# Kernel optimization log

Measured on AMD Instinct MI355X. Metric: run time of the kernel, lower is better.

## Reference

```python
import jax, jax.numpy as jnp
import numpy as np

B, TQ, TK, D, NA = 8, 512, 2048, 1024, 512
H, HD = 16, 64          # n_head, head_dim (D = H*HD)
NE, HID = 4, 32         # n_experts, expert hidden_dim
EPS = 1e-6


def _rmsnorm(x, w):
    return x * jax.lax.rsqrt(jnp.mean(x * x, axis=-1, keepdims=True) + EPS) * w


def setup_inputs() -> dict:
    key = jax.random.key(0)
    ks = jax.random.split(key, 20)
    r = lambda i, shp: jax.random.normal(ks[i], shp, dtype=jnp.float32) * 0.02
    return {
        'q': jax.random.normal(ks[0], (B, TQ, D), dtype=jnp.float32),
        'kv': jax.random.normal(ks[1], (B, TK, D), dtype=jnp.float32),
        'qn_w': jnp.ones((D,), jnp.float32),
        'kva_w': jnp.ones((D,), jnp.float32),
        'kvi_w': jnp.ones((D,), jnp.float32),
        'dn_w': jnp.ones((D,), jnp.float32),
        'fn_w': jnp.ones((D,), jnp.float32),
        'Wq': r(2, (D, D)), 'bq': jnp.zeros((D,), jnp.float32),
        'Wk': r(3, (D, D)), 'bk': jnp.zeros((D,), jnp.float32),
        'Wv': r(4, (D, D)), 'bv': jnp.zeros((D,), jnp.float32),
        'Wo': r(5, (D, D)), 'bo': jnp.zeros((D,), jnp.float32),
        'active_bias': r(6, (D,)),
        'inactive_bias': r(7, (D,)),
        'log_temp': jnp.array(0.0, jnp.float32),
        'gate_attn': jnp.array(0.3, jnp.float32),
        'gate_ffn': jnp.array(0.7, jnp.float32),
        'Wr': r(8, (D, NE)), 'br': jnp.zeros((NE,), jnp.float32),
        'W1': r(9, (NE, D, 2 * HID)), 'b1': jnp.zeros((NE, 2 * HID), jnp.float32),
        'W2': r(10, (NE, HID, D)), 'b2': jnp.zeros((NE, D), jnp.float32),
        'kv_mask': jnp.ones((B, TK), bool),
        'n_actives': NA,
    }


def _forward(q, kv, qn_w, kva_w, kvi_w, dn_w, fn_w,
             Wq, bq, Wk, bk, Wv, bv, Wo, bo,
             active_bias, inactive_bias, log_temp, gate_attn, gate_ffn,
             Wr, br, W1, b1, W2, b2, kv_mask, n_actives):
    Na = int(n_actives)
    Tk = kv.shape[1]
    Ni = Tk - Na
    b, tq, d = q.shape

    # split-normed kv, with active/inactive learned biases injected pre-KV-proj
    kv_a = _rmsnorm(kv[:, :Na], kva_w) + active_bias
    kv_i = _rmsnorm(kv[:, Na:], kvi_w) + inactive_bias
    kv_b = jnp.concatenate([kv_a, kv_i], axis=1)

    qn = _rmsnorm(q, qn_w)
    qp = (qn @ Wq + bq).reshape(b, tq, H, HD).transpose(0, 2, 1, 3)  # (B,H,Tq,hd)
    k = (kv_b @ Wk + bk).reshape(b, Tk, H, HD).transpose(0, 2, 1, 3)
    v = (kv_b @ Wv + bv).reshape(b, Tk, H, HD).transpose(0, 2, 1, 3)

    # torch: q *= 1/sqrt(hd), then SDPA(q/temp, ...) applies another 1/sqrt(hd)
    temp = jnp.clip(jnp.exp(log_temp), 0.1, 10.0)
    scale = 1.0 / (HD * temp)

    def attn(kk, vv):
        logits = jnp.einsum('bhqd,bhkd->bhqk', qp, kk) * scale
        return jnp.einsum('bhqk,bhkd->bhqd', jax.nn.softmax(logits, axis=-1), vv)

    out = attn(k[:, :, :Na], v[:, :, :Na]) / np.sqrt(max(Na, 1)) \
        - attn(k[:, :, Na:], v[:, :, Na:]) / np.sqrt(max(Ni, 1))
    out = out.transpose(0, 2, 1, 3).reshape(b, tq, d)
    delta = _rmsnorm(out @ Wo + bo, dn_w)
    q_new = q + jax.nn.sigmoid(gate_attn) * delta

    # dense soft MoE over normed kv, with query-similarity logit bias
    x = _rmsnorm(kv, fn_w)
    logits = x @ Wr + br                                   # (B,Tk,NE)
    q_vec = jnp.mean(q_new, axis=1, keepdims=True)         # (B,1,D)
    sim = jnp.einsum('bqd,btd->bt', q_vec, x)              # (B,Tk)
    probs = jax.nn.softmax(logits + sim[..., None], axis=-1)

    h = jnp.einsum('btd,edh->bteh', x, W1) + b1            # (B,Tk,NE,2*HID)
    xp, g = h[..., :HID], h[..., HID:]
    act = xp * (g * jax.nn.sigmoid(g))                     # SwiGLU
    eo = jnp.einsum('bteh,ehd->bted', act, W2) + b2        # (B,Tk,NE,D)
    moe_out = jnp.einsum('bte,bted->btd', probs, eo)

    kv_new = kv + jax.nn.sigmoid(gate_ffn) * moe_out
    return q_new, kv_new


def reference(q, kv, qn_w, kva_w, kvi_w, dn_w, fn_w,
              Wq, bq, Wk, bk, Wv, bv, Wo, bo,
              active_bias, inactive_bias, log_temp, gate_attn, gate_ffn,
              Wr, br, W1, b1, W2, b2, kv_mask, n_actives):
    return _forward(q, kv, qn_w, kva_w, kvi_w, dn_w, fn_w,
                    Wq, bq, Wk, bk, Wv, bv, Wo, bo,
                    active_bias, inactive_bias, log_temp, gate_attn, gate_ffn,
                    Wr, br, W1, b1, W2, b2, kv_mask, n_actives)
```

## Files before the change

kernel.cpp:

```cpp
#include <hip/hip_runtime.h>
#include <hip/hip_bf16.h>
#include <stdint.h>


#define B_   8
#define TQ_  512
#define TK_  2048
#define D_   1024
#define H_   16
#define HD_  64
#define NE_  4
#define HID_ 32
#define EPSF 1e-6f
#define LOG2E 1.44269504f

typedef __bf16 bf16_t;
typedef __bf16 bf16x8 __attribute__((ext_vector_type(8)));
typedef __bf16 bf16x4 __attribute__((ext_vector_type(4)));
typedef float  f32x4  __attribute__((ext_vector_type(4)));

typedef __attribute__((address_space(1))) void gvoid_t;
typedef __attribute__((address_space(3))) void lvoid_t;

__device__ __forceinline__ void gld_lds16(const void* g, void* l) {
  __builtin_amdgcn_global_load_lds((gvoid_t*)g, (lvoid_t*)l, 16, 0, 0);
}

struct TP2 { const float* in[2]; bf16_t* out[2]; };

__global__ void transpose_conv2_kernel(TP2 p) {
  __shared__ float tile[32][33];
  const int bz = blockIdx.z;
  const float* in = p.in[bz];
  bf16_t* out = p.out[bz];
  const int rb = blockIdx.y * 32, cb = blockIdx.x * 32;
  const int txi = threadIdx.x, tyi = threadIdx.y;
#pragma unroll
  for (int i = 0; i < 32; i += 8)
    tile[tyi + i][txi] = in[(size_t)(rb + tyi + i) * D_ + cb + txi];
  __syncthreads();
#pragma unroll
  for (int i = 0; i < 32; i += 8)
    out[(size_t)(cb + tyi + i) * D_ + rb + txi] = (bf16_t)tile[txi][tyi + i];
}

__global__ void transpose_fragorder_kernel(TP2 p) {
  __shared__ float tile[32][33];
  const float* in = p.in[blockIdx.z];
  bf16_t* out = p.out[blockIdx.z];
  const int kb0 = blockIdx.y * 32;
  const int nb0 = blockIdx.x * 32;
  const int tx = threadIdx.x, ty = threadIdx.y;
#pragma unroll
  for (int i = 0; i < 32; i += 8)
    tile[ty + i][tx] = in[(size_t)(kb0 + ty + i) * D_ + nb0 + tx];
  __syncthreads();
  const int t = ty * 32 + tx;
  const int n_l = t >> 3;
  const int k_l = (t & 7) * 4;
  const int n = nb0 + n_l;
  const int k = kb0 + k_l;
  const int tile_n = n >> 7, rn = n & 127, hc = rn >> 6, rr = rn & 63;
  const int j = rr >> 4, l15 = rr & 15;
  const int s = k >> 5, lg = (k >> 3) & 3, e = k & 7;
  bf16x4 o;
#pragma unroll
  for (int c = 0; c < 4; ++c) o[c] = (bf16_t)tile[k_l + c][n_l];
  *(bf16x4*)&out[(size_t)tile_n * 131072 + s * 4096 + hc * 2048 +
                 j * 512 + (lg * 16 + l15) * 8 + e] = o;
}

__global__ void transpose_conv_kernel(const float* __restrict__ in, bf16_t* __restrict__ out,
                                      int R, int C, int in_bstride,
                                      int out_rstride, int ob_row, int ob_col) {
  __shared__ float tile[32][33];
  const int bz = blockIdx.z;
  const int rb = blockIdx.y * 32, cb = blockIdx.x * 32;
  const int txi = threadIdx.x, tyi = threadIdx.y;
  const float* inp = in + (size_t)bz * in_bstride;
#pragma unroll
  for (int i = 0; i < 32; i += 8) {
    const int r = rb + tyi + i, c = cb + txi;
    if (r < R && c < C) tile[tyi + i][txi] = inp[(size_t)r * C + c];
  }
  __syncthreads();
#pragma unroll
  for (int i = 0; i < 32; i += 8) {
    const int orow = cb + tyi + i;
    const int ocol = rb + txi;
    if (orow < C && ocol < R)
      out[(size_t)(orow + bz * ob_row) * out_rstride + bz * ob_col + ocol] =
          (bf16_t)tile[txi][tyi + i];
  }
}

__device__ __forceinline__ float block_rsum(float v, float* red) {
  v += __shfl_xor(v, 1);  v += __shfl_xor(v, 2);  v += __shfl_xor(v, 4);
  v += __shfl_xor(v, 8);  v += __shfl_xor(v, 16); v += __shfl_xor(v, 32);
  const int tid = threadIdx.x;
  if ((tid & 63) == 0) red[tid >> 6] = v;
  __syncthreads();
  return red[0] + red[1] + red[2] + red[3];
}

__global__ __launch_bounds__(256)
void rms_kv_kernel(const float* __restrict__ kv, const float* __restrict__ kva_w,
                   const float* __restrict__ kvi_w, const float* __restrict__ fn_w,
                   const float* __restrict__ ab, const float* __restrict__ ib,
                   const int* __restrict__ n_act, const float* __restrict__ Wr,
                   const float* __restrict__ br,
                   bf16_t* __restrict__ kvb, bf16_t* __restrict__ xn,
                   float* __restrict__ probs) {
  __shared__ float red[4];
  __shared__ f32x4 pred[4];
  const int row = blockIdx.x;
  const int t = row & (TK_ - 1);
  const int tid = threadIdx.x;
  const float* src = kv + (size_t)row * D_;
  f32x4 v = ((const f32x4*)src)[tid];
  float ss = v[0]*v[0] + v[1]*v[1] + v[2]*v[2] + v[3]*v[3];
  ss = block_rsum(ss, red);
  const float rs = rsqrtf(ss * (1.0f / D_) + EPSF);
  const int Na = n_act[0];
  const float* wsel = (t < Na) ? kva_w : kvi_w;
  const float* bsel = (t < Na) ? ab : ib;
  const int d = tid * 4;
  f32x4 wv = *(const f32x4*)(wsel + d);
  f32x4 bv = *(const f32x4*)(bsel + d);
  f32x4 fv = *(const f32x4*)(fn_w + d);
  bf16x4 o0, o1;
  f32x4 p4 = {};
#pragma unroll
  for (int c = 0; c < 4; ++c) {
    const float xv = v[c] * rs;
    const float xf = xv * fv[c];
    o0[c] = (bf16_t)(xv * wv[c] + bv[c]);
    o1[c] = (bf16_t)xf;
    const f32x4 w4 = *(const f32x4*)&Wr[(d + c) * 4];
    p4 += w4 * xf;
  }
  {
    const int rl = row & 127, hh = rl >> 6, rr2 = rl & 63;
    const int ii = rr2 >> 4, l15 = rr2 & 15;
    const int s2 = d >> 5, lg2 = (d >> 3) & 3, e2 = d & 7;
    *(bf16x4*)&kvb[(size_t)(row >> 7) * 131072 + s2 * 4096 + hh * 2048 +
                   ii * 512 + (lg2 * 16 + l15) * 8 + e2] = o0;
  }
  *(bf16x4*)&xn[(size_t)row * D_ + d] = o1;
#pragma unroll
  for (int m = 1; m <= 32; m <<= 1) {
    p4[0] += __shfl_xor(p4[0], m); p4[1] += __shfl_xor(p4[1], m);
    p4[2] += __shfl_xor(p4[2], m); p4[3] += __shfl_xor(p4[3], m);
  }
  if ((tid & 63) == 0) pred[tid >> 6] = p4;
  __syncthreads();
  if (tid == 0) {
    f32x4 s = pred[0] + pred[1] + pred[2] + pred[3];
    s[0] += br[0]; s[1] += br[1]; s[2] += br[2]; s[3] += br[3];
    const float mx = fmaxf(fmaxf(s[0], s[1]), fmaxf(s[2], s[3]));
    const float e0 = __expf(s[0] - mx), e1 = __expf(s[1] - mx);
    const float e2 = __expf(s[2] - mx), e3 = __expf(s[3] - mx);
    const float inv = 1.0f / (e0 + e1 + e2 + e3);
    f32x4 pr = { e0 * inv, e1 * inv, e2 * inv, e3 * inv };
    *(f32x4*)&probs[row * 4] = pr;
  }
}

__global__ __launch_bounds__(256)
void rms_q_kernel(const float* __restrict__ q, const float* __restrict__ qn_w,
                  bf16_t* __restrict__ qn) {
  __shared__ float red[4];
  const int row = blockIdx.x;
  const int tid = threadIdx.x;
  const float* src = q + (size_t)row * D_;
  f32x4 v = ((const f32x4*)src)[tid];
  float ss = v[0]*v[0] + v[1]*v[1] + v[2]*v[2] + v[3]*v[3];
  ss = block_rsum(ss, red);
  const float rs = rsqrtf(ss * (1.0f / D_) + EPSF);
  const int d = tid * 4;
  f32x4 wv = *(const f32x4*)(qn_w + d);
  bf16x4 o0;
#pragma unroll
  for (int c = 0; c < 4; ++c) o0[c] = (bf16_t)(v[c] * rs * wv[c]);
  *(bf16x4*)&qn[(size_t)row * D_ + d] = o0;
}

__device__ __forceinline__ int xcd_swz(int bx, int gx) {
  if ((gx & 7) == 0) { const int cpx = gx >> 3; return (bx & 7) * cpx + (bx >> 3); }
  return bx;
}

__global__ __launch_bounds__(256)
void gemm_kv(const bf16_t* __restrict__ A, const bf16_t* __restrict__ Wk,
             const bf16_t* __restrict__ Wv, const float* __restrict__ bk,
             const float* __restrict__ bv, bf16_t* __restrict__ Kout,
             bf16_t* __restrict__ Vt) {
  __shared__ alignas(16) bf16_t lds[3 * 8192];
  bf16_t* As  = lds;
  bf16_t* Bks = lds + 8192;
  bf16_t* Bvs = lds + 16384;
  const int tid = threadIdx.x;
  const int lane = tid & 63;
  const int w = tid >> 6;
  const int wr = w >> 1, wc = w & 1;
  const int lane15 = lane & 15, lgrp = lane >> 4;

  const int flat = blockIdx.x;
  const int xcd = flat & 7;
  const int local = flat >> 3;
  const int tg = local >> 3;
  const int yy = local & 7;
  const int m0 = (xcd * 16 + tg) * 128;
  const int n0 = yy * 128;

  f32x4 acc_k[4][4] = {};
  f32x4 acc_v[4][4] = {};

  const bf16_t* ga = A  + (size_t)(m0 >> 7) * 131072 + tid * 8;
  const bf16_t* gk = Wk + (size_t)(n0 >> 7) * 131072 + tid * 8;
  const bf16_t* gv = Wv + (size_t)(n0 >> 7) * 131072 + tid * 8;

  auto STAGE = [&](int s, int bufi) {
    const int off = bufi * 4096;
    const size_t so = (size_t)s * 4096;
    gld_lds16(ga + so,        &As [off + tid * 8]);
    gld_lds16(ga + so + 2048, &As [off + 2048 + tid * 8]);
    gld_lds16(gk + so,        &Bks[off + tid * 8]);
    gld_lds16(gk + so + 2048, &Bks[off + 2048 + tid * 8]);
    gld_lds16(gv + so,        &Bvs[off + tid * 8]);
    gld_lds16(gv + so + 2048, &Bvs[off + 2048 + tid * 8]);
  };

  STAGE(0, 0);
  int buf = 0;
  const int abase0 = wr * 2048 + lane * 8;
  const int bbase0 = wc * 2048 + lane * 8;
  for (int s = 0; s < 32; ++s) {
    __syncthreads();
    if (s + 1 < 32) STAGE(s + 1, buf ^ 1);
    const int off = buf * 4096;
    bf16x8 af[4], bkf[4], bvf[4];
#pragma unroll
    for (int i = 0; i < 4; ++i) af[i]  = *(const bf16x8*)&As [off + abase0 + i * 512];
#pragma unroll
    for (int j = 0; j < 4; ++j) bkf[j] = *(const bf16x8*)&Bks[off + bbase0 + j * 512];
#pragma unroll
    for (int j = 0; j < 4; ++j) bvf[j] = *(const bf16x8*)&Bvs[off + bbase0 + j * 512];
    __builtin_amdgcn_s_setprio(1);
#pragma unroll
    for (int i = 0; i < 4; ++i)
#pragma unroll
      for (int j = 0; j < 4; ++j) {
        acc_k[i][j] = __builtin_amdgcn_mfma_f32_16x16x32_bf16(af[i], bkf[j], acc_k[i][j], 0, 0, 0);
        acc_v[i][j] = __builtin_amdgcn_mfma_f32_16x16x32_bf16(af[i], bvf[j], acc_v[i][j], 0, 0, 0);
      }
    __builtin_amdgcn_s_setprio(0);
    buf ^= 1;
  }

  const int row0 = m0 + wr * 64 + (lgrp << 2);
  const int col0 = n0 + wc * 64 + lane15;
#pragma unroll
  for (int j = 0; j < 4; ++j) {
    const int cc = col0 + j * 16;
    const float bkv = bk[cc];
#pragma unroll
    for (int i = 0; i < 4; ++i) {
      const int rr = row0 + i * 16;
#pragma unroll
      for (int r = 0; r < 4; ++r)
        Kout[(size_t)(rr + r) * D_ + cc] = (bf16_t)(acc_k[i][j][r] + bkv);
    }
  }

  __syncthreads();
  bf16_t* vt_l = lds + w * 4608;
#pragma unroll
  for (int j = 0; j < 4; ++j) {
    const int nl = j * 16 + lane15;
    const float bvv = bv[n0 + wc * 64 + nl];
#pragma unroll
    for (int i = 0; i < 4; ++i) {
      bf16x4 pv;
#pragma unroll
      for (int r = 0; r < 4; ++r) pv[r] = (bf16_t)(acc_v[i][j][r] + bvv);
      *(bf16x4*)&vt_l[nl * 72 + i * 16 + lgrp * 4] = pv;
    }
  }
  const int bidx2 = m0 >> 11;
  const int tok0 = (m0 & (TK_ - 1)) + wr * 64;
  bf16_t* vbase = Vt + (size_t)bidx2 * D_ * TK_ + (size_t)(n0 + wc * 64) * TK_ + tok0;
#pragma unroll
  for (int it = 0; it < 8; ++it) {
    const int ln = (lane >> 3) + it * 8;
    const int tk = (lane & 7) * 8;
    const bf16x8 v8 = *(const bf16x8*)&vt_l[ln * 72 + tk];
    *(bf16x8*)&vbase[(size_t)ln * TK_ + tk] = v8;
  }
}

__device__ __forceinline__ void gemm_loop_db(const bf16_t* __restrict__ ga,
                                             const bf16_t* __restrict__ gb,
                                             bf16_t* As, bf16_t* Bs, int K,
                                             size_t rstep, int ar, int br2,
                                             int tid, f32x4 acc[4][4]) {
  gld_lds16(ga,         &As[tid * 8]);
  gld_lds16(ga + rstep, &As[2048 + tid * 8]);
  gld_lds16(gb,         &Bs[tid * 8]);
  gld_lds16(gb + rstep, &Bs[2048 + tid * 8]);
  int buf = 0;
  for (int k0 = 0; k0 < K; k0 += 32) {
    __syncthreads();
    if (k0 + 32 < K) {
      const int nb = buf ^ 1;
      gld_lds16(ga + k0 + 32,         &As[nb * 4096 + tid * 8]);
      gld_lds16(ga + k0 + 32 + rstep, &As[nb * 4096 + 2048 + tid * 8]);
      gld_lds16(gb + k0 + 32,         &Bs[nb * 4096 + tid * 8]);
      gld_lds16(gb + k0 + 32 + rstep, &Bs[nb * 4096 + 2048 + tid * 8]);
    }
    bf16x8 af[4], bfr[4];
#pragma unroll
    for (int i = 0; i < 4; ++i) af[i]  = *(const bf16x8*)&As[buf * 4096 + ar  + i * 512];
#pragma unroll
    for (int j = 0; j < 4; ++j) bfr[j] = *(const bf16x8*)&Bs[buf * 4096 + br2 + j * 512];
#pragma unroll
    for (int i = 0; i < 4; ++i)
#pragma unroll
      for (int j = 0; j < 4; ++j)
        acc[i][j] = __builtin_amdgcn_mfma_f32_16x16x32_bf16(af[i], bfr[j], acc[i][j], 0, 0, 0);
    buf ^= 1;
  }
}

__device__ __forceinline__ void gemm64_loop_db(const bf16_t* __restrict__ ga,
                                               const bf16_t* __restrict__ gb,
                                               bf16_t* As, bf16_t* Bs, int K,
                                               size_t rstep, int ar, int br2,
                                               int tid, f32x4 acc[2][4]) {
  gld_lds16(ga,         &As[tid * 8]);
  gld_lds16(gb,         &Bs[tid * 8]);
  gld_lds16(gb + rstep, &Bs[2048 + tid * 8]);
  int buf = 0;
  for (int k0 = 0; k0 < K; k0 += 32) {
    __syncthreads();
    if (k0 + 32 < K) {
      const int nb = buf ^ 1;
      gld_lds16(ga + k0 + 32,         &As[nb * 2048 + tid * 8]);
      gld_lds16(gb + k0 + 32,         &Bs[nb * 4096 + tid * 8]);
      gld_lds16(gb + k0 + 32 + rstep, &Bs[nb * 4096 + 2048 + tid * 8]);
    }
    bf16x8 af[2], bfr[4];
#pragma unroll
    for (int i = 0; i < 2; ++i) af[i]  = *(const bf16x8*)&As[buf * 2048 + ar  + i * 512];
#pragma unroll
    for (int j = 0; j < 4; ++j) bfr[j] = *(const bf16x8*)&Bs[buf * 4096 + br2 + j * 512];
#pragma unroll
    for (int i = 0; i < 2; ++i)
#pragma unroll
      for (int j = 0; j < 4; ++j)
        acc[i][j] = __builtin_amdgcn_mfma_f32_16x16x32_bf16(af[i], bfr[j], acc[i][j], 0, 0, 0);
    buf ^= 1;
  }
}

template<int HAS_BIAS>
__global__ __launch_bounds__(256)
void gemm64_tn(const bf16_t* __restrict__ A, const bf16_t* __restrict__ Wt,
               const float* __restrict__ bias, bf16_t* __restrict__ C,
               int M, int N, int K) {
  __shared__ alignas(16) bf16_t As[2 * 64 * 32];
  __shared__ alignas(16) bf16_t Bs[2 * 128 * 32];
  const int tid = threadIdx.x;
  const int lane = tid & 63;
  const int w = tid >> 6;
  const int wr = w >> 1, wc = w & 1;
  const int m0 = xcd_swz(blockIdx.x, gridDim.x) * 64;
  const int n0 = blockIdx.y * 128;

  f32x4 acc[2][4] = {};
  const bf16_t* ga = A  + (size_t)(m0 + (tid >> 2)) * K + (tid & 3) * 8;
  const bf16_t* gb = Wt + (size_t)(n0 + (tid >> 2)) * K + (tid & 3) * 8;
  const int kb = (lane >> 4) * 8;
  const int ar  = ((wr * 32 + (lane & 15)) << 5) + kb;
  const int br2 = ((wc * 64 + (lane & 15)) << 5) + kb;

  gemm64_loop_db(ga, gb, As, Bs, K, (size_t)64 * K, ar, br2, tid, acc);

  const int row0 = m0 + wr * 32 + ((lane >> 4) << 2);
  const int col0 = n0 + wc * 64 + (lane & 15);
#pragma unroll
  for (int j = 0; j < 4; ++j) {
    const int cc = col0 + j * 16;
    const float bv = HAS_BIAS ? bias[cc] : 0.0f;
#pragma unroll
    for (int i = 0; i < 2; ++i) {
      const int rr = row0 + i * 16;
#pragma unroll
      for (int r = 0; r < 4; ++r)
        C[(size_t)(rr + r) * N + cc] = (bf16_t)(acc[i][j][r] + bv);
    }
  }
}

__global__ __launch_bounds__(256)
void gemm64_h_act(const bf16_t* __restrict__ A, const bf16_t* __restrict__ Wt,
                  const float* __restrict__ bias, const float* __restrict__ probs,
                  bf16_t* __restrict__ a2) {
  __shared__ alignas(16) bf16_t As[2 * 64 * 32];
  __shared__ alignas(16) bf16_t Bs[2 * 128 * 32];
  const int K = D_;
  const int tid = threadIdx.x;
  const int lane = tid & 63;
  const int w = tid >> 6;
  const int wr = w >> 1, wc = w & 1;
  const int m0 = xcd_swz(blockIdx.x, gridDim.x) * 64;
  const int n0 = blockIdx.y * 128;

  f32x4 acc[2][4] = {};
  const bf16_t* ga = A  + (size_t)(m0 + (tid >> 2)) * K + (tid & 3) * 8;
  const bf16_t* gb = Wt + (size_t)(n0 + (tid >> 2)) * K + (tid & 3) * 8;
  const int kb = (lane >> 4) * 8;
  const int ar  = ((wr * 32 + (lane & 15)) << 5) + kb;
  const int br2 = ((wc * 64 + (lane & 15)) << 5) + kb;

  gemm64_loop_db(ga, gb, As, Bs, K, (size_t)64 * K, ar, br2, tid, acc);

  const int row0 = m0 + wr * 32 + ((lane >> 4) << 2);
  const int hbase = n0 + wc * 64 + (lane & 15);
  const int e = hbase >> 6;
#pragma unroll
  for (int j = 0; j < 2; ++j) {
    const int ch = hbase + j * 16;
    const float bx = bias[ch], bg = bias[ch + 32];
    const int ac = (ch & 63) + e * 32;
#pragma unroll
    for (int i = 0; i < 2; ++i) {
      const int rr = row0 + i * 16;
#pragma unroll
      for (int r = 0; r < 4; ++r) {
        const float xp = acc[i][j][r] + bx;
        const float g  = acc[i][j + 2][r] + bg;
        const float sg = 1.0f / (1.0f + __expf(-g));
        const float pr = probs[(size_t)(rr + r) * 4 + e];
        a2[(size_t)(rr + r) * 128 + ac] = (bf16_t)(pr * xp * g * sg);
      }
    }
  }
}

__global__ __launch_bounds__(256)
void gemm_moe_kvnew(const bf16_t* __restrict__ A, const bf16_t* __restrict__ Wt,
                    const float* __restrict__ kv, const float* __restrict__ probs,
                    const float* __restrict__ b2, const float* __restrict__ gate_ffn,
                    float* __restrict__ out) {
  __shared__ alignas(16) bf16_t As[2 * 128 * 32];
  __shared__ alignas(16) bf16_t Bs[2 * 128 * 32];
  const int K = 128, N = D_;
  const int tid = threadIdx.x;
  const int lane = tid & 63;
  const int w = tid >> 6;
  const int wr = w >> 1, wc = w & 1;
  const int m0 = xcd_swz(blockIdx.x, gridDim.x) * 128;
  const int n0 = blockIdx.y * 128;

  f32x4 acc[4][4] = {};
  const bf16_t* ga = A  + (size_t)(m0 + (tid >> 2)) * K + (tid & 3) * 8;
  const bf16_t* gb = Wt + (size_t)(n0 + (tid >> 2)) * K + (tid & 3) * 8;
  const int kb = (lane >> 4) * 8;
  const int ar  = ((wr * 64 + (lane & 15)) << 5) + kb;
  const int br2 = ((wc * 64 + (lane & 15)) << 5) + kb;

  gemm_loop_db(ga, gb, As, Bs, K, (size_t)64 * K, ar, br2, tid, acc);

  const float sgf = 1.0f / (1.0f + __expf(-gate_ffn[0]));
  const int row0 = m0 + wr * 64 + ((lane >> 4) << 2);
  const int col0 = n0 + wc * 64 + (lane & 15);
#pragma unroll
  for (int j = 0; j < 4; ++j) {
    const int cc = col0 + j * 16;
    const f32x4 b2v = { b2[0 * D_ + cc], b2[1 * D_ + cc], b2[2 * D_ + cc], b2[3 * D_ + cc] };
#pragma unroll
    for (int i = 0; i < 4; ++i) {
      const int rr = row0 + i * 16;
#pragma unroll
      for (int r = 0; r < 4; ++r) {
        const f32x4 pr = *(const f32x4*)&probs[(size_t)(rr + r) * 4];
        const float bsum = pr[0]*b2v[0] + pr[1]*b2v[1] + pr[2]*b2v[2] + pr[3]*b2v[3];
        out[(size_t)(rr + r) * N + cc] =
            kv[(size_t)(rr + r) * N + cc] + sgf * (acc[i][j][r] + bsum);
      }
    }
  }
}

__global__ __launch_bounds__(128, 2)
void attn_mfma_kernel(const bf16_t* __restrict__ qp, const bf16_t* __restrict__ kb,
                      const bf16_t* __restrict__ vt, bf16_t* __restrict__ attno,
                      const float* __restrict__ log_temp, const int* __restrict__ n_act) {
  __shared__ alignas(16) bf16_t Ks[2][64 * 64];
  __shared__ alignas(16) bf16_t Vs[2][64 * 64];
  __shared__ alignas(16) bf16_t Ps[2][32 * 64];

  const int dd = blockIdx.x;
  const int xcd = dd & 7, within = dd >> 3;
  const int qt = within & 7, slot0 = within >> 3;
  const int bh = slot0 * 8 + xcd;
  const int b = bh >> 4, h = bh & 15;

  const int tid = threadIdx.x;
  const int lane = tid & 63;
  const int w = tid >> 6;
  const int lane15 = lane & 15, lgrp = lane >> 4, l7 = lane & 7;
  const int Na = n_act[0];
  float temp = __expf(log_temp[0]);
  temp = fminf(fmaxf(temp, 0.1f), 10.0f);
  const float lsc = LOG2E / (64.0f * temp);
  const int rowbase = qt * 64 + w * 32;

  const bf16_t* qsrcA = qp + (size_t)(b * TQ_ + rowbase + lane15) * D_ + h * 64 + lgrp * 8;
  const bf16_t* qsrcB = qsrcA + (size_t)16 * D_;
  bf16x8 qfA0 = *(const bf16x8*)qsrcA;
  bf16x8 qfA1 = *(const bf16x8*)(qsrcA + 32);
  bf16x8 qfB0 = *(const bf16x8*)qsrcB;
  bf16x8 qfB1 = *(const bf16x8*)(qsrcB + 32);
#pragma unroll
  for (int j = 0; j < 8; ++j) {
    qfA0[j] = (bf16_t)((float)qfA0[j] * lsc);
    qfA1[j] = (bf16_t)((float)qfA1[j] * lsc);
    qfB0[j] = (bf16_t)((float)qfB0[j] * lsc);
    qfB1[j] = (bf16_t)((float)qfB1[j] * lsc);
  }

  const int srow = tid >> 3;
  const int schunk = (tid & 7) ^ (srow & 7);
  const bf16_t* ksrc = kb + (size_t)(b * TK_ + srow) * D_ + h * 64 + schunk * 8;
  const bf16_t* vsrc = vt + ((size_t)(b * 16 + h) * 64 + srow) * TK_ + schunk * 8;

  f32x4 oA[4] = {}, oB[4] = {}, outA[4] = {}, outB[4] = {};
  float laccA = 0.f, laccB = 0.f;

  const float inv_sa = rsqrtf((float)(Na > 1 ? Na : 1));
  const int Ni = TK_ - Na;
  const float inv_si = rsqrtf((float)(Ni > 1 ? Ni : 1));

#pragma unroll
  for (int r = 0; r < 4; ++r) {
    gld_lds16(ksrc + (size_t)r * 16 * D_, &Ks[0][r * 1024 + tid * 8]);
    gld_lds16(vsrc + (size_t)r * 16 * TK_, &Vs[0][r * 1024 + tid * 8]);
  }

  for (int t = 0; t < TK_ / 64; ++t) {
    const int cur = t & 1;
    __syncthreads();
    if (t + 1 < TK_ / 64) {
      const int nb = cur ^ 1;
      const bf16_t* kN = ksrc + (size_t)(t + 1) * 64 * D_;
      const bf16_t* vN = vsrc + (size_t)(t + 1) * 64;
#pragma unroll
      for (int r = 0; r < 4; ++r) {
        gld_lds16(kN + (size_t)r * 16 * D_, &Ks[nb][r * 1024 + tid * 8]);
        gld_lds16(vN + (size_t)r * 16 * TK_, &Vs[nb][r * 1024 + tid * 8]);
      }
    }

    f32x4 sA[4], sB[4];
    __builtin_amdgcn_s_setprio(1);
#pragma unroll
    for (int cf = 0; cf < 4; ++cf) {
      const int krow = (cf * 16 + lane15) * 64;
      const bf16x8 kf0 = *(const bf16x8*)&Ks[cur][krow + ((lgrp ^ l7) << 3)];
      const bf16x8 kf1 = *(const bf16x8*)&Ks[cur][krow + (((lgrp + 4) ^ l7) << 3)];
      f32x4 s = {};
      s = __builtin_amdgcn_mfma_f32_16x16x32_bf16(kf0, qfA0, s, 0, 0, 0);
      s = __builtin_amdgcn_mfma_f32_16x16x32_bf16(kf1, qfA1, s, 0, 0, 0);
      sA[cf] = s;
      f32x4 s2 = {};
      s2 = __builtin_amdgcn_mfma_f32_16x16x32_bf16(kf0, qfB0, s2, 0, 0, 0);
      s2 = __builtin_amdgcn_mfma_f32_16x16x32_bf16(kf1, qfB1, s2, 0, 0, 0);
      sB[cf] = s2;
    }
    __builtin_amdgcn_s_setprio(0);

#pragma unroll
    for (int cf = 0; cf < 4; ++cf) {
      const int c = cf * 2 + (lgrp >> 1);
      const int pcol = ((c ^ l7) << 3) + (lgrp & 1) * 4;
      f32x4 pA, pB;
#pragma unroll
      for (int r = 0; r < 4; ++r) pA[r] = exp2f(sA[cf][r]);
#pragma unroll
      for (int r = 0; r < 4; ++r) pB[r] = exp2f(sB[cf][r]);
      laccA += (pA[0] + pA[1]) + (pA[2] + pA[3]);
      laccB += (pB[0] + pB[1]) + (pB[2] + pB[3]);
      bf16x4 pvA, pvB;
#pragma unroll
      for (int r = 0; r < 4; ++r) { pvA[r] = (bf16_t)pA[r]; pvB[r] = (bf16_t)pB[r]; }
      *(bf16x4*)&Ps[w][lane15 * 64 + pcol]        = pvA;
      *(bf16x4*)&Ps[w][(16 + lane15) * 64 + pcol] = pvB;
    }

    {
      const int prowA = lane15 * 64;
      const int prowB = (16 + lane15) * 64;
      const bf16x8 paA0 = *(const bf16x8*)&Ps[w][prowA + ((lgrp ^ l7) << 3)];
      const bf16x8 paA1 = *(const bf16x8*)&Ps[w][prowA + (((lgrp + 4) ^ l7) << 3)];
      const bf16x8 paB0 = *(const bf16x8*)&Ps[w][prowB + ((lgrp ^ l7) << 3)];
      const bf16x8 paB1 = *(const bf16x8*)&Ps[w][prowB + (((lgrp + 4) ^ l7) << 3)];
      __builtin_amdgcn_s_setprio(1);
#pragma unroll
      for (int df = 0; df < 4; ++df) {
        const int vrow = (df * 16 + lane15) * 64;
        const bf16x8 vf0 = *(const bf16x8*)&Vs[cur][vrow + ((lgrp ^ l7) << 3)];
        const bf16x8 vf1 = *(const bf16x8*)&Vs[cur][vrow + (((lgrp + 4) ^ l7) << 3)];
        oA[df] = __builtin_amdgcn_mfma_f32_16x16x32_bf16(paA0, vf0, oA[df], 0, 0, 0);
        oA[df] = __builtin_amdgcn_mfma_f32_16x16x32_bf16(paA1, vf1, oA[df], 0, 0, 0);
        oB[df] = __builtin_amdgcn_mfma_f32_16x16x32_bf16(paB0, vf0, oB[df], 0, 0, 0);
        oB[df] = __builtin_amdgcn_mfma_f32_16x16x32_bf16(paB1, vf1, oB[df], 0, 0, 0);
      }
      __builtin_amdgcn_s_setprio(0);
    }

    const bool endA = ((t + 1) * 64 == Na);
    const bool endI = (t == TK_ / 64 - 1);
    if (endA || endI) {
      float lA = laccA, lB = laccB;
      lA += __shfl_xor(lA, 16); lA += __shfl_xor(lA, 32);
      lB += __shfl_xor(lB, 16); lB += __shfl_xor(lB, 32);
      const float ssc = endA ? inv_sa : -inv_si;
      f32x4 ivA, ivB;
#pragma unroll
      for (int r = 0; r < 4; ++r) {
        ivA[r] = ssc / __shfl(lA, lgrp * 4 + r);
        ivB[r] = ssc / __shfl(lB, lgrp * 4 + r);
      }
#pragma unroll
      for (int df = 0; df < 4; ++df) {
        outA[df] += oA[df] * ivA; oA[df] = (f32x4){};
        outB[df] += oB[df] * ivB; oB[df] = (f32x4){};
      }
      laccA = 0.f; laccB = 0.f;
    }
  }

#pragma unroll
  for (int df = 0; df < 4; ++df)
#pragma unroll
    for (int r = 0; r < 4; ++r) {
      const size_t ro = (size_t)(b * TQ_ + rowbase + lgrp * 4 + r) * D_ + h * 64 + df * 16 + lane15;
      attno[ro]           = (bf16_t)outA[df][r];
      attno[ro + 16 * D_] = (bf16_t)outB[df][r];
    }
}

__global__ __launch_bounds__(256)
void delta_qnew_kernel(const bf16_t* __restrict__ proj, const float* __restrict__ dn_w,
                       const float* __restrict__ q, const float* __restrict__ gate_attn,
                       float* __restrict__ qnew) {
  __shared__ float red[4];
  const int row = blockIdx.x;
  const int tid = threadIdx.x;
  bf16x4 pv = *(const bf16x4*)(proj + (size_t)row * D_ + tid * 4);
  f32x4 v;
#pragma unroll
  for (int c = 0; c < 4; ++c) v[c] = (float)pv[c];
  float ss = v[0]*v[0] + v[1]*v[1] + v[2]*v[2] + v[3]*v[3];
  ss = block_rsum(ss, red);
  const float rs = rsqrtf(ss * (1.0f / D_) + EPSF);
  const float sga = 1.0f / (1.0f + __expf(-gate_attn[0]));
  const int d = tid * 4;
  f32x4 wv = *(const f32x4*)(dn_w + d);
  f32x4 qv = *(const f32x4*)(q + (size_t)row * D_ + d);
  f32x4 out;
#pragma unroll
  for (int c = 0; c < 4; ++c) out[c] = qv[c] + sga * (v[c] * rs * wv[c]);
  *(f32x4*)&qnew[(size_t)row * D_ + d] = out;
}

extern "C" void kernel_launch(void* const* d_in, const int* in_sizes, int n_in,
                              void* d_out, int out_size, void* d_ws, size_t ws_size,
                              hipStream_t stream) {
  const float* q           = (const float*)d_in[0];
  const float* kv          = (const float*)d_in[1];
  const float* qn_w        = (const float*)d_in[2];
  const float* kva_w       = (const float*)d_in[3];
  const float* kvi_w       = (const float*)d_in[4];
  const float* dn_w        = (const float*)d_in[5];
  const float* fn_w        = (const float*)d_in[6];
  const float* Wq          = (const float*)d_in[7];
  const float* bq          = (const float*)d_in[8];
  const float* Wk          = (const float*)d_in[9];
  const float* bk          = (const float*)d_in[10];
  const float* Wv          = (const float*)d_in[11];
  const float* bv          = (const float*)d_in[12];
  const float* Wo          = (const float*)d_in[13];
  const float* bo          = (const float*)d_in[14];
  const float* active_bias = (const float*)d_in[15];
  const float* inactive_b  = (const float*)d_in[16];
  const float* log_temp    = (const float*)d_in[17];
  const float* gate_attn   = (const float*)d_in[18];
  const float* gate_ffn    = (const float*)d_in[19];
  const float* Wr          = (const float*)d_in[20];
  const float* br          = (const float*)d_in[21];
  const float* W1          = (const float*)d_in[22];
  const float* b1          = (const float*)d_in[23];
  const float* W2          = (const float*)d_in[24];
  const float* b2          = (const float*)d_in[25];
  const int*   n_act       = (const int*)d_in[27];

  char* ws = (char*)d_ws;
  size_t off = 0;
  auto alloc = [&](size_t bytes) -> char* {
    char* p = ws + off;
    off = (off + bytes + 255) & ~(size_t)255;
    return p;
  };

  bf16_t* wqT  = (bf16_t*)alloc((size_t)D_ * D_ * 2);
  bf16_t* wkT  = (bf16_t*)alloc((size_t)D_ * D_ * 2);
  bf16_t* wvT  = (bf16_t*)alloc((size_t)D_ * D_ * 2);
  bf16_t* woT  = (bf16_t*)alloc((size_t)D_ * D_ * 2);
  bf16_t* w1T  = (bf16_t*)alloc((size_t)256 * D_ * 2);
  bf16_t* w2T  = (bf16_t*)alloc((size_t)D_ * 128 * 2);
  bf16_t* kvb  = (bf16_t*)alloc((size_t)B_ * TK_ * D_ * 2);
  bf16_t* xn   = (bf16_t*)alloc((size_t)B_ * TK_ * D_ * 2);
  bf16_t* qn   = (bf16_t*)alloc((size_t)B_ * TQ_ * D_ * 2);
  bf16_t* qp   = (bf16_t*)alloc((size_t)B_ * TQ_ * D_ * 2);
  bf16_t* kbuf = (bf16_t*)alloc((size_t)B_ * TK_ * D_ * 2);
  bf16_t* vt   = (bf16_t*)alloc((size_t)B_ * D_ * TK_ * 2);
  float*  probs = (float*)alloc((size_t)B_ * TK_ * NE_ * 4);
  bf16_t* attno = qn;
  bf16_t* proj  = qp;
  bf16_t* a2buf = kbuf;
  (void)ws_size; (void)in_sizes; (void)n_in; (void)out_size;

  float* q_new_out  = (float*)d_out;
  float* kv_new_out = (float*)d_out + (size_t)B_ * TQ_ * D_;

  dim3 tb(32, 8);
  TP2 tpa; tpa.in[0] = Wq; tpa.in[1] = Wo; tpa.out[0] = wqT; tpa.out[1] = woT;
  transpose_conv2_kernel<<<dim3(32, 32, 2), tb, 0, stream>>>(tpa);
  TP2 tpf; tpf.in[0] = Wk; tpf.in[1] = Wv; tpf.out[0] = wkT; tpf.out[1] = wvT;
  transpose_fragorder_kernel<<<dim3(32, 32, 2), tb, 0, stream>>>(tpf);
  transpose_conv_kernel<<<dim3(2, 32, 4), tb, 0, stream>>>(W1, w1T, D_, 64, D_ * 64, D_, 64, 0);
  transpose_conv_kernel<<<dim3(32, 1, 4), tb, 0, stream>>>(W2, w2T, 32, D_, 32 * D_, 128, 0, 32);

  rms_kv_kernel<<<B_ * TK_, 256, 0, stream>>>(kv, kva_w, kvi_w, fn_w, active_bias,
                                              inactive_b, n_act, Wr, br, kvb, xn, probs);
  rms_q_kernel<<<B_ * TQ_, 256, 0, stream>>>(q, qn_w, qn);

  gemm64_tn<1><<<dim3(B_ * TQ_ / 64, D_ / 128), 256, 0, stream>>>(qn, wqT, bq, qp, B_ * TQ_, D_, D_);
  gemm_kv<<<B_ * TK_ / 128 * (D_ / 128), 256, 0, stream>>>(kvb, wkT, wvT, bk, bv, kbuf, vt);

  attn_mfma_kernel<<<B_ * H_ * (TQ_ / 64), 128, 0, stream>>>(qp, kbuf, vt, attno, log_temp, n_act);

  gemm64_tn<1><<<dim3(B_ * TQ_ / 64, D_ / 128), 256, 0, stream>>>(attno, woT, bo, proj, B_ * TQ_, D_, D_);
  delta_qnew_kernel<<<B_ * TQ_, 256, 0, stream>>>(proj, dn_w, q, gate_attn, q_new_out);

  gemm64_h_act<<<dim3(B_ * TK_ / 64, 2), 256, 0, stream>>>(xn, w1T, b1, probs, a2buf);
  gemm_moe_kvnew<<<dim3(B_ * TK_ / 128, D_ / 128), 256, 0, stream>>>(a2buf, w2T, kv, probs, b2,
                                                                     gate_ffn, kv_new_out);
}
```

Measured before the change: 352.0 us.

## Triple-buffer the KV projection GEMM with explicit vmcnt waits

Switches the fused K/V projection GEMM from double buffering to a three-stage LDS ring, keeping two stages of global-to-LDS loads in flight. A partial `s_waitcnt vmcnt` plus a raw barrier replaces the full `__syncthreads`. The next stage's loads are issued after the LDS fragment reads rather than before them. The aim is to hide more global-load latency behind the MFMA work; the cost is LDS growing from 48KB to 72KB per block, which can lower occupancy.

```diff
diff --git a/kernel.cpp b/kernel.cpp
--- a/kernel.cpp
+++ b/kernel.cpp
@@ -195,10 +195,7 @@
              const bf16_t* __restrict__ Wv, const float* __restrict__ bk,
              const float* __restrict__ bv, bf16_t* __restrict__ Kout,
              bf16_t* __restrict__ Vt) {
-  __shared__ alignas(16) bf16_t lds[3 * 8192];
-  bf16_t* As  = lds;
-  bf16_t* Bks = lds + 8192;
-  bf16_t* Bvs = lds + 16384;
+  __shared__ alignas(16) bf16_t lds[3 * 12288];
   const int tid = threadIdx.x;
   const int lane = tid & 63;
   const int w = tid >> 6;
@@ -220,32 +217,36 @@
   const bf16_t* gk = Wk + (size_t)(n0 >> 7) * 131072 + tid * 8;
   const bf16_t* gv = Wv + (size_t)(n0 >> 7) * 131072 + tid * 8;
 
-  auto STAGE = [&](int s, int bufi) {
-    const int off = bufi * 4096;
+  auto STAGE = [&](int s) {
+    bf16_t* dst = lds + (s % 3) * 12288 + tid * 8;
     const size_t so = (size_t)s * 4096;
-    gld_lds16(ga + so,        &As [off + tid * 8]);
-    gld_lds16(ga + so + 2048, &As [off + 2048 + tid * 8]);
-    gld_lds16(gk + so,        &Bks[off + tid * 8]);
-    gld_lds16(gk + so + 2048, &Bks[off + 2048 + tid * 8]);
-    gld_lds16(gv + so,        &Bvs[off + tid * 8]);
-    gld_lds16(gv + so + 2048, &Bvs[off + 2048 + tid * 8]);
+    gld_lds16(ga + so,        dst);
+    gld_lds16(ga + so + 2048, dst + 2048);
+    gld_lds16(gk + so,        dst + 4096);
+    gld_lds16(gk + so + 2048, dst + 6144);
+    gld_lds16(gv + so,        dst + 8192);
+    gld_lds16(gv + so + 2048, dst + 10240);
   };
 
-  STAGE(0, 0);
-  int buf = 0;
-  const int abase0 = wr * 2048 + lane * 8;
-  const int bbase0 = wc * 2048 + lane * 8;
+  STAGE(0);
+  STAGE(1);
+
+  const int abase = wr * 2048 + lane * 8;
+  const int bbase = wc * 2048 + lane * 8;
   for (int s = 0; s < 32; ++s) {
-    __syncthreads();
-    if (s + 1 < 32) STAGE(s + 1, buf ^ 1);
-    const int off = buf * 4096;
+    if (s < 30) asm volatile("s_waitcnt vmcnt(6)" ::: "memory");
+    else        asm volatile("s_waitcnt vmcnt(0)" ::: "memory");
+    __builtin_amdgcn_s_barrier();
+    __builtin_amdgcn_sched_barrier(0);
+    const bf16_t* buf = lds + (s % 3) * 12288;
     bf16x8 af[4], bkf[4], bvf[4];
 #pragma unroll
-    for (int i = 0; i < 4; ++i) af[i]  = *(const bf16x8*)&As [off + abase0 + i * 512];
-#pragma unroll
-    for (int j = 0; j < 4; ++j) bkf[j] = *(const bf16x8*)&Bks[off + bbase0 + j * 512];
-#pragma unroll
-    for (int j = 0; j < 4; ++j) bvf[j] = *(const bf16x8*)&Bvs[off + bbase0 + j * 512];
+    for (int i = 0; i < 4; ++i) af[i]  = *(const bf16x8*)&buf[abase + i * 512];
+#pragma unroll
+    for (int j = 0; j < 4; ++j) bkf[j] = *(const bf16x8*)&buf[4096 + bbase + j * 512];
+#pragma unroll
+    for (int j = 0; j < 4; ++j) bvf[j] = *(const bf16x8*)&buf[8192 + bbase + j * 512];
+    if (s + 2 < 32) STAGE(s + 2);
     __builtin_amdgcn_s_setprio(1);
 #pragma unroll
     for (int i = 0; i < 4; ++i)
@@ -255,7 +256,6 @@
         acc_v[i][j] = __builtin_amdgcn_mfma_f32_16x16x32_bf16(af[i], bvf[j], acc_v[i][j], 0, 0, 0);
       }
     __builtin_amdgcn_s_setprio(0);
-    buf ^= 1;
   }
 
   const int row0 = m0 + wr * 64 + (lgrp << 2);
```

After: 330.4 us. -6.1%, faster.
